# Performance work log

Hardware: AMD Instinct MI355X
Metric: run time of the kernel (lower is better)

## Reference

```python
import jax, jax.numpy as jnp
from jax import lax
import numpy as np

B, C, H, W = 16, 256, 96, 96
K = 11            # conv kernel size along one axis
C8 = C // 8       # query/key channels


def _conv(x, w, b):
    # 'same' conv in NCHW with OIHW weights; kernel is (kh,1) or (1,kw)
    kh, kw = w.shape[2], w.shape[3]
    y = lax.conv_general_dilated(
        x, w, window_strides=(1, 1),
        padding=((kh // 2, kh // 2), (kw // 2, kw // 2)),
        dimension_numbers=('NCHW', 'OIHW', 'NCHW'))
    return y + b[None, :, None, None]


def setup_inputs() -> dict:
    key = jax.random.key(0)
    ks = jax.random.split(key, 14)
    s = 0.05
    d = {
        'x':    jax.random.normal(ks[0], (B, C, H, W), jnp.float32),
        'wq_h': jax.random.normal(ks[1], (C8, C, K, 1), jnp.float32) * s,
        'bq_h': jax.random.normal(ks[2], (C8,), jnp.float32) * s,
        'wq_w': jax.random.normal(ks[3], (C8, C, 1, K), jnp.float32) * s,
        'bq_w': jax.random.normal(ks[4], (C8,), jnp.float32) * s,
        'wk_h': jax.random.normal(ks[5], (C8, C, K, 1), jnp.float32) * s,
        'bk_h': jax.random.normal(ks[6], (C8,), jnp.float32) * s,
        'wk_w': jax.random.normal(ks[7], (C8, C, 1, K), jnp.float32) * s,
        'bk_w': jax.random.normal(ks[8], (C8,), jnp.float32) * s,
        'wv_h': jax.random.normal(ks[9], (C, C, K, 1), jnp.float32) * s,
        'bv_h': jax.random.normal(ks[10], (C,), jnp.float32) * s,
        'wv_w': jax.random.normal(ks[11], (C, C, 1, K), jnp.float32) * s,
        'bv_w': jax.random.normal(ks[12], (C,), jnp.float32) * s,
        # gamma is a learned scalar (zero-init in torch); nonzero here so the
        # attention path contributes to the output
        'gamma': jax.random.normal(ks[13], (1,), jnp.float32) * 0.5,
    }
    return d


def reference(x, wq_h, bq_h, wq_w, bq_w, wk_h, bk_h, wk_w, bk_w,
              wv_h, bv_h, wv_w, bv_w, gamma):
    b, c, h, w = x.shape
    q_h = _conv(x, wq_h, bq_h)   # [B, C8, H, W]
    q_w = _conv(x, wq_w, bq_w)
    k_h = _conv(x, wk_h, bk_h)
    k_w = _conv(x, wk_w, bk_w)
    v_h = _conv(x, wv_h, bv_h)   # [B, C, H, W]
    v_w = _conv(x, wv_w, bv_w)
    # column (H-axis) attention energies: [B, H, W, H'] with -inf on h==h'
    e_h = jnp.einsum('bchw,bcHw->bhwH', q_h, k_h)
    diag = jnp.eye(h, dtype=bool)[None, :, None, :]  # [1, H, 1, H']
    e_h = jnp.where(diag, -jnp.inf, e_h)
    # row (W-axis) attention energies: [B, H, W, W']
    e_w = jnp.einsum('bchw,bchW->bhwW', q_w, k_w)
    # joint softmax over concatenated H'+W' axis
    att = jax.nn.softmax(jnp.concatenate([e_h, e_w], axis=-1), axis=-1)
    a_h = att[..., :h]           # [B, H, W, H']
    a_w = att[..., h:]           # [B, H, W, W']
    out_h = jnp.einsum('bcHw,bhwH->bchw', v_h, a_h)
    out_w = jnp.einsum('bchW,bhwW->bchw', v_w, a_w)
    return gamma * (out_h + out_w) + x
```

## Files before the change

### kernel.cpp

```cpp
#include <hip/hip_runtime.h>

constexpr int Bn = 16, Cn = 256, Hn = 96, Wn = 96, Pn = Hn * Wn;

#define DI static __device__ __forceinline__

struct alignas(16) U4 { unsigned a, b, c, d; };

typedef _Float16 f16x8 __attribute__((ext_vector_type(8)));
typedef float f32x4 __attribute__((ext_vector_type(4)));

#define GLOAD16(g, l) __builtin_amdgcn_global_load_lds( \
    (const __attribute__((address_space(1))) void*)(g), \
    (__attribute__((address_space(3))) void*)(l), 16, 0, 0)

__global__ void k_wt16(const float* __restrict__ w, _Float16* __restrict__ wt,
                       int co_n, int co_off, int co_tot) {
    int idx = blockIdx.x * 256 + threadIdx.x;
    if (idx >= co_n * 2816) return;
    int co = idx / 2816;
    int r  = idx - co * 2816;
    int c  = r / 11, t = r - c * 11;
    wt[((size_t)t * co_tot + co_off + co) * 256 + c] = (_Float16)w[idx];
}

__global__ __launch_bounds__(256) void k_xsplit(const float* __restrict__ x,
                                                _Float16* __restrict__ xh, _Float16* __restrict__ xl,
                                                _Float16* __restrict__ xhT, _Float16* __restrict__ xlT) {
    int b = blockIdx.y;
    int tid = threadIdx.x;
    int p = blockIdx.x * 128 + (tid >> 1);
    int half = tid & 1;
    int h = p / 96, w = p - h * 96;
    int pT = w * 96 + h;
    const float* xb = x + (size_t)b * Cn * Pn + p;
    size_t ob  = ((size_t)b * Pn + p) * 256;
    size_t obT = ((size_t)b * Pn + pT) * 256;
    for (int it = 0; it < 16; ++it) {
        int c0 = it * 16 + half * 8;
        f16x8 vh_, vl_;
#pragma unroll
        for (int i = 0; i < 8; ++i) {
            float f = xb[(size_t)(c0 + i) * Pn];
            _Float16 hh = (_Float16)f;
            vh_[i] = hh;
            vl_[i] = (_Float16)(f - (float)hh);
        }
        *(f16x8*)(xh + ob + c0) = vh_;
        *(f16x8*)(xl + ob + c0) = vl_;
        *(f16x8*)(xhT + obT + c0) = vh_;
        *(f16x8*)(xlT + obT + c0) = vl_;
    }
}

__global__ __launch_bounds__(256, 2) void k_conv_v(const _Float16* __restrict__ X0,
                                                   const _Float16* __restrict__ W0,
                                                   const float* __restrict__ b0a,
                                                   _Float16* __restrict__ o0,
                                                   const _Float16* __restrict__ X1,
                                                   const _Float16* __restrict__ W1,
                                                   const float* __restrict__ b1a,
                                                   _Float16* __restrict__ o1) {
    __shared__ char sm_raw[57344];
    const int tid = threadIdx.x;
    const int lane = tid & 63, wave = tid >> 6;
    const int wm = wave >> 1, wn = wave & 1;
    const int l15 = lane & 15, kg = lane >> 4;
    int fid = blockIdx.x + 24 * (blockIdx.y + 4 * blockIdx.z);
    int swz = (fid & 7) * 384 + (fid >> 3);
    const int bx = swz % 24;
    int rest = swz / 24;
    const int co0 = (rest & 3) * 64;
    const int z = rest >> 2;
    const int fam = z >> 4, b = z & 15;
    const _Float16* X  = fam ? X1 : X0;
    const _Float16* WT = fam ? W1 : W0;
    const float* bias  = fam ? b1a : b0a;
    _Float16* out      = fam ? o1 : o0;

    for (int zz = tid; zz < 2048; zz += 256) {
        int bufo = (zz >> 10) * 28672;
        int s = (zz >> 7) & 7, off = zz & 127;
        int Rbase = (s >> 1) * 112 + ((s & 1) ? 104 : 0);
        *(unsigned*)(sm_raw + bufo + Rbase * 64 + off * 4) = 0u;
    }

    f32x4 acc[2][12];
#pragma unroll
    for (int mf = 0; mf < 2; ++mf) {
        const float* bp = bias + co0 + wm * 32 + mf * 16 + kg * 4;
        f32x4 bv = { bp[0], bp[1], bp[2], bp[3] };
#pragma unroll
        for (int j = 0; j < 12; ++j) acc[mf][j] = bv;
    }

    const _Float16* Xb = X + ((size_t)b * Pn + bx * 384) * 256;
    const _Float16* Wb = WT + (size_t)(co0 + wm * 32 + l15) * 256 + kg * 8;

    auto STAGE = [&](int c0, int bufo) {
        for (int i = wave; i < 24; i += 4) {
            int s = i / 6, wch = i - s * 6;
            int row_local = 8 + wch * 16 + (lane >> 2);
            int kchunk = (lane & 3) ^ ((row_local >> 1) & 3);
            const _Float16* src = Xb + ((size_t)(s * 96 + row_local - 8)) * 256 + c0 + kchunk * 8;
            char* dst = sm_raw + bufo + (s * 112 + 8 + wch * 16) * 64;
            GLOAD16(src, dst);
        }
    };
    auto LDA = [&](f16x8* slot, const _Float16* tp) {
#pragma unroll
        for (int mf = 0; mf < 2; ++mf) slot[mf] = *(const f16x8*)(tp + mf * 4096);
    };
    auto LDB = [&](f16x8* dst, const char* Bb, int T) {
        int rl0 = 3 + l15 + T;
        const char* bp = Bb + (wn * 224 + rl0) * 64 + ((kg ^ ((rl0 >> 1) & 3)) << 4);
#pragma unroll
        for (int s = 0; s < 2; ++s)
#pragma unroll
            for (int nf = 0; nf < 6; ++nf)
                dst[s * 6 + nf] = *(const f16x8*)(bp + s * 7168 + nf * 1024);
    };

    STAGE(0, 0);
    __syncthreads();

    int cur = 0;
    for (int s8 = 0; s8 < 8; ++s8) {
        const int c0 = s8 * 32;
        const _Float16* wc = Wb + c0;
        f16x8 afc[2], afn[2];
        LDA(afc, wc);
        if (s8 < 7) STAGE(c0 + 32, (cur ^ 1) * 28672);
        const char* Bb = sm_raw + cur * 28672;
        f16x8 bf[12];
#pragma unroll
        for (int t = 0; t < 11; ++t) {
            if (t < 10) LDA(afn, wc + (t + 1) * 65536);
            LDB(bf, Bb, t);
            __builtin_amdgcn_s_setprio(1);
#pragma unroll
            for (int mf = 0; mf < 2; ++mf)
#pragma unroll
                for (int j = 0; j < 12; ++j)
                    acc[mf][j] = __builtin_amdgcn_mfma_f32_16x16x32_f16(afc[mf], bf[j], acc[mf][j], 0, 0, 0);
            __builtin_amdgcn_s_setprio(0);
            if (t < 10) {
#pragma unroll
                for (int mf = 0; mf < 2; ++mf) afc[mf] = afn[mf];
            }
        }
        __syncthreads();
        cur ^= 1;
    }

    _Float16* sb = (_Float16*)sm_raw;
#pragma unroll
    for (int mf = 0; mf < 2; ++mf)
#pragma unroll
        for (int j = 0; j < 12; ++j)
#pragma unroll
            for (int r = 0; r < 4; ++r) {
                int row = wm * 32 + mf * 16 + kg * 4 + r;
                int p = wn * 192 + (j / 6) * 96 + (j % 6) * 16 + l15;
                sb[row * 384 + p] = (_Float16)acc[mf][j][r];
            }
    __syncthreads();
    for (int k = 0; k < 12; ++k) {
        int ci = tid + k * 256;
        int row = ci / 48, ch = ci - row * 48;
        U4 v = *(const U4*)(sm_raw + row * 768 + ch * 16);
        *(U4*)(out + ((size_t)b * 256 + co0 + row) * Pn + bx * 384 + ch * 8) = v;
    }
}

__global__ __launch_bounds__(256, 2) void k_conv_qk(const _Float16* __restrict__ Xh0,
                                                    const _Float16* __restrict__ Xl0,
                                                    const _Float16* __restrict__ W0,
                                                    const float* __restrict__ bq0, const float* __restrict__ bk0,
                                                    _Float16* __restrict__ q0, _Float16* __restrict__ k0,
                                                    const _Float16* __restrict__ Xh1,
                                                    const _Float16* __restrict__ Xl1,
                                                    const _Float16* __restrict__ W1,
                                                    const float* __restrict__ bq1, const float* __restrict__ bk1,
                                                    _Float16* __restrict__ q1, _Float16* __restrict__ k1) {
    __shared__ char sm_raw[57344];
    const int tid = threadIdx.x;
    const int lane = tid & 63, wave = tid >> 6;
    const int wm = wave >> 1, wn = wave & 1;
    const int l15 = lane & 15, kg = lane >> 4;
    int fid = blockIdx.x + 48 * blockIdx.z;
    int swz = (fid & 7) * 192 + (fid >> 3);
    const int bx = swz % 48;
    const int zz0 = swz / 48;
    const int fam = zz0 >> 4, b = zz0 & 15;
    const _Float16* Xh = fam ? Xh1 : Xh0;
    const _Float16* Xl = fam ? Xl1 : Xl0;
    const _Float16* WT = fam ? W1 : W0;
    const float* bq = fam ? bq1 : bq0;
    const float* bk = fam ? bk1 : bk0;
    _Float16* q16 = fam ? q1 : q0;
    _Float16* k16 = fam ? k1 : k0;

    for (int z = tid; z < 2048; z += 256) {
        int bufo = (z >> 10) * 28672;
        int s = (z >> 7) & 7, off = z & 127;
        int Rbase = (s >> 1) * 112 + ((s & 1) ? 104 : 0);
        *(unsigned*)(sm_raw + bufo + Rbase * 64 + off * 4) = 0u;
    }

    f32x4 acc[2][6];
#pragma unroll
    for (int mf = 0; mf < 2; ++mf) {
        int cb = wm * 32 + mf * 16 + kg * 4;
        f32x4 bv;
#pragma unroll
        for (int r = 0; r < 4; ++r) {
            int co_l = cb + r;
            bv[r] = (co_l < 32) ? bq[co_l] : bk[co_l - 32];
        }
#pragma unroll
        for (int nf = 0; nf < 6; ++nf) acc[mf][nf] = bv;
    }

    const _Float16* Xbh = Xh + ((size_t)b * Pn + bx * 192) * 256;
    const _Float16* Xbl = Xl + ((size_t)b * Pn + bx * 192) * 256;
    const _Float16* Wb = WT + (size_t)(wm * 32 + l15) * 256 + kg * 8;

    auto STAGE = [&](int c0, int bufo) {
        for (int i = wave; i < 24; i += 4) {
            int a = i / 12, rr = (i / 6) & 1, wch = i % 6;
            int row_local = 8 + wch * 16 + (lane >> 2);
            int kchunk = (lane & 3) ^ ((row_local >> 1) & 3);
            const _Float16* base = (a == 0) ? Xbh : Xbl;
            const _Float16* src = base + ((size_t)(rr * 96 + row_local - 8)) * 256 + c0 + kchunk * 8;
            char* dst = sm_raw + bufo + ((a * 2 + rr) * 112 + 8 + wch * 16) * 64;
            GLOAD16(src, dst);
        }
    };
    auto LDBHL = [&](f16x8* dh, f16x8* dl, const char* Bb, int T) {
        int rl0 = 3 + l15 + T;
        const char* bp = Bb + (wn * 112 + rl0) * 64 + ((kg ^ ((rl0 >> 1) & 3)) << 4);
#pragma unroll
        for (int nf = 0; nf < 6; ++nf) {
            dh[nf] = *(const f16x8*)(bp + nf * 1024);
            dl[nf] = *(const f16x8*)(bp + 14336 + nf * 1024);
        }
    };

    STAGE(0, 0);
    __syncthreads();

    int cur = 0;
    for (int s8 = 0; s8 < 8; ++s8) {
        const int c0 = s8 * 32;
        const _Float16* wc = Wb + c0;
        f16x8 afc[2], afn[2];
#pragma unroll
        for (int mf = 0; mf < 2; ++mf) afc[mf] = *(const f16x8*)(wc + mf * 4096);
        if (s8 < 7) STAGE(c0 + 32, (cur ^ 1) * 28672);
        const char* Bb = sm_raw + cur * 28672;
#pragma unroll
        for (int t = 0; t < 11; ++t) {
            if (t < 10) {
#pragma unroll
                for (int mf = 0; mf < 2; ++mf)
                    afn[mf] = *(const f16x8*)(wc + (t + 1) * 16384 + mf * 4096);
            }
            f16x8 bh[6], bl[6];
            LDBHL(bh, bl, Bb, t);
            __builtin_amdgcn_s_setprio(1);
#pragma unroll
            for (int mf = 0; mf < 2; ++mf)
#pragma unroll
                for (int nf = 0; nf < 6; ++nf) {
                    acc[mf][nf] = __builtin_amdgcn_mfma_f32_16x16x32_f16(afc[mf], bh[nf], acc[mf][nf], 0, 0, 0);
                    acc[mf][nf] = __builtin_amdgcn_mfma_f32_16x16x32_f16(afc[mf], bl[nf], acc[mf][nf], 0, 0, 0);
                }
            __builtin_amdgcn_s_setprio(0);
            if (t < 10) {
#pragma unroll
                for (int mf = 0; mf < 2; ++mf) afc[mf] = afn[mf];
            }
        }
        __syncthreads();
        cur ^= 1;
    }

    __syncthreads();
    _Float16* sq = (_Float16*)sm_raw;
    _Float16* sk = (_Float16*)(sm_raw + 12288);
#pragma unroll
    for (int mf = 0; mf < 2; ++mf) {
        int cb = wm * 32 + mf * 16 + kg * 4;
#pragma unroll
        for (int r = 0; r < 4; ++r) {
            int co_l = cb + r;
            _Float16* arr = (co_l < 32) ? sq : sk;
            int c = co_l & 31;
#pragma unroll
            for (int nf = 0; nf < 6; ++nf) {
                int p = wn * 96 + nf * 16 + l15;
                arr[p * 32 + c] = (_Float16)acc[mf][nf][r];
            }
        }
    }
    __syncthreads();
    for (int j = 0; j < 6; ++j) {
        int idx = tid + j * 256;
        int mtx = idx >= 768;
        int e = idx - mtx * 768;
        int p = e >> 2, cg2 = e & 3;
        U4 v = *(const U4*)(sm_raw + mtx * 12288 + p * 64 + cg2 * 16);
        _Float16* dstb = mtx ? k16 : q16;
        *(U4*)(dstb + ((size_t)b * Pn + bx * 192 + p) * 32 + cg2 * 8) = v;
    }
}

DI void stage_qk16(const _Float16* qg, const _Float16* kg, char* Lq, char* Lk, int tid) {
    for (int i = tid; i < 768; i += 256) {
        int mtx = i >= 384;
        int e = i - mtx * 384;
        int p = e >> 2, ch = e & 3;
        const _Float16* src = (mtx ? kg : qg) + p * 32 + ch * 8;
        f16x8 v = *(const f16x8*)src;
        char* dst = (mtx ? Lk : Lq) + p * 64 + ((ch ^ ((p >> 1) & 3)) << 4);
        *(f16x8*)dst = v;
    }
}

DI void mfma_e(const char* Lq, const char* Lk, float* Ef, int lane, int wave) {
    int l15 = lane & 15, kg = lane >> 4;
    int wm = wave >> 1, wn = wave & 1;
    f16x8 qa[3], kb[3];
#pragma unroll
    for (int i = 0; i < 3; ++i) {
        int pr = wm * 48 + i * 16 + l15;
        qa[i] = *(const f16x8*)(Lq + pr * 64 + ((kg ^ ((pr >> 1) & 3)) << 4));
        int pc = wn * 48 + i * 16 + l15;
        kb[i] = *(const f16x8*)(Lk + pc * 64 + ((kg ^ ((pc >> 1) & 3)) << 4));
    }
#pragma unroll
    for (int i = 0; i < 3; ++i)
#pragma unroll
        for (int j = 0; j < 3; ++j) {
            f32x4 a = { 0.f, 0.f, 0.f, 0.f };
            a = __builtin_amdgcn_mfma_f32_16x16x32_f16(qa[i], kb[j], a, 0, 0, 0);
#pragma unroll
            for (int r = 0; r < 4; ++r) {
                int row = wm * 48 + i * 16 + kg * 4 + r;
                int col = wn * 48 + j * 16 + l15;
                Ef[row * 97 + col] = a[r];
            }
        }
}

__global__ __launch_bounds__(256) void k_p1(const _Float16* __restrict__ q16, const _Float16* __restrict__ k16,
                                            float* __restrict__ mh, float* __restrict__ lh) {
    __shared__ char L[49536];
    float* Ef = (float*)L;
    char* Lq = L + 37248;
    char* Lk = L + 43392;
    const int tid = threadIdx.x, lane = tid & 63, wave = tid >> 6;
    const int w = blockIdx.x, b = blockIdx.y;
    const _Float16* qg = q16 + ((size_t)b * Pn + w * 96) * 32;
    const _Float16* kg = k16 + ((size_t)b * Pn + w * 96) * 32;
    stage_qk16(qg, kg, Lq, Lk, tid);
    __syncthreads();
    mfma_e(Lq, Lk, Ef, lane, wave);
    __syncthreads();
    if (tid < 96) {
        int h = tid;
        const float* er = Ef + h * 97;
        float m = -INFINITY;
        for (int j = 0; j < 96; ++j) if (j != h) m = fmaxf(m, er[j]);
        float l = 0.f;
        for (int j = 0; j < 96; ++j) if (j != h) l += __expf(er[j] - m);
        mh[((size_t)b * 96 + w) * 96 + h] = m;
        lh[((size_t)b * 96 + w) * 96 + h] = l;
    }
}

__global__ __launch_bounds__(256) void k_p2(const _Float16* __restrict__ q16, const _Float16* __restrict__ k16,
                                            const _Float16* __restrict__ V,
                                            const float* __restrict__ mh, const float* __restrict__ lh,
                                            float* __restrict__ mo, float* __restrict__ lo,
                                            _Float16* __restrict__ outw) {
    __shared__ char L[56448];
    float* Ef = (float*)L;
    char* LA  = L + 37248;
    char* Lq  = L + 37248;
    char* Lk  = L + 43392;
    float* Marr = (float*)(L + 55680);
    float* Linv = (float*)(L + 56064);
    const int tid = threadIdx.x, lane = tid & 63, wave = tid >> 6;
    const int l15 = lane & 15, kg = lane >> 4;
    const int h = blockIdx.x, b = blockIdx.y;
    const _Float16* qg = q16 + ((size_t)b * Pn + h * 96) * 32;
    const _Float16* kgp = k16 + ((size_t)b * Pn + h * 96) * 32;
    stage_qk16(qg, kgp, Lq, Lk, tid);
    __syncthreads();
    mfma_e(Lq, Lk, Ef, lane, wave);
    __syncthreads();
    if (tid < 96) {
        int wq = tid;
        const float* er = Ef + wq * 97;
        float mw = -INFINITY;
        for (int j = 0; j < 96; ++j) mw = fmaxf(mw, er[j]);
        float lw = 0.f;
        for (int j = 0; j < 96; ++j) lw += __expf(er[j] - mw);
        float mhv = mh[((size_t)b * 96 + wq) * 96 + h];
        float lhv = lh[((size_t)b * 96 + wq) * 96 + h];
        float m = fmaxf(mhv, mw);
        float l = lhv * __expf(mhv - m) + lw * __expf(mw - m);
        mo[((size_t)b * 96 + h) * 96 + wq] = m;
        lo[((size_t)b * 96 + h) * 96 + wq] = l;
        Marr[wq] = m;
        Linv[wq] = 1.f / l;
    }
    __syncthreads();
    if (tid < 192) {
        int r = tid >> 1, half = tid & 1;
        float m = Marr[r], li = Linv[r];
        const float* er = Ef + r * 97;
        for (int cc = 0; cc < 6; ++cc) {
            int chunk = half * 6 + cc;
            f16x8 av;
#pragma unroll
            for (int jj = 0; jj < 8; ++jj)
                av[jj] = (_Float16)(__expf(er[chunk * 8 + jj] - m) * li);
            *(f16x8*)(LA + r * 192 + ((chunk ^ ((r >> 1) & 3)) << 4)) = av;
        }
    }
    __syncthreads();
    f32x4 acc[4][6];
#pragma unroll
    for (int mf = 0; mf < 4; ++mf)
#pragma unroll
        for (int nf = 0; nf < 6; ++nf) acc[mf][nf] = f32x4{ 0.f, 0.f, 0.f, 0.f };
    const _Float16* vb = V + ((size_t)b * 256 + wave * 64 + l15) * Pn + h * 96 + kg * 8;
    f16x8 va[4][3];
#pragma unroll
    for (int mf = 0; mf < 4; ++mf)
#pragma unroll
        for (int ks = 0; ks < 3; ++ks)
            va[mf][ks] = *(const f16x8*)(vb + (size_t)mf * 16 * Pn + ks * 32);
#pragma unroll
    for (int ks = 0; ks < 3; ++ks)
#pragma unroll
        for (int nf = 0; nf < 6; ++nf) {
            int wq = nf * 16 + l15;
            int chunk = ks * 4 + kg;
            f16x8 bv = *(const f16x8*)(LA + wq * 192 + ((chunk ^ ((wq >> 1) & 3)) << 4));
#pragma unroll
            for (int mf = 0; mf < 4; ++mf)
                acc[mf][nf] = __builtin_amdgcn_mfma_f32_16x16x32_f16(va[mf][ks], bv, acc[mf][nf], 0, 0, 0);
        }
    _Float16* ob = outw + ((size_t)b * 256) * Pn + h * 96;
#pragma unroll
    for (int mf = 0; mf < 4; ++mf)
#pragma unroll
        for (int nf = 0; nf < 6; ++nf)
#pragma unroll
            for (int r = 0; r < 4; ++r) {
                int c = wave * 64 + mf * 16 + kg * 4 + r;
                ob[(size_t)c * Pn + nf * 16 + l15] = (_Float16)acc[mf][nf][r];
            }
}

__global__ __launch_bounds__(256) void k_p3(const _Float16* __restrict__ q16, const _Float16* __restrict__ k16,
                                            const _Float16* __restrict__ V,
                                            const float* __restrict__ mo, const float* __restrict__ lo,
                                            _Float16* __restrict__ pT) {
    __shared__ char L[56448];
    float* Ef = (float*)L;
    char* LA  = L + 37248;
    char* Lq  = L + 37248;
    char* Lk  = L + 43392;
    float* Marr = (float*)(L + 55680);
    float* Linv = (float*)(L + 56064);
    const int tid = threadIdx.x, lane = tid & 63, wave = tid >> 6;
    const int l15 = lane & 15, kg = lane >> 4;
    const int w = blockIdx.x, b = blockIdx.y;
    const _Float16* qg = q16 + ((size_t)b * Pn + w * 96) * 32;
    const _Float16* kgp = k16 + ((size_t)b * Pn + w * 96) * 32;
    stage_qk16(qg, kgp, Lq, Lk, tid);
    __syncthreads();
    mfma_e(Lq, Lk, Ef, lane, wave);
    __syncthreads();
    if (tid < 96) {
        int hq = tid;
        Marr[hq] = mo[((size_t)b * 96 + hq) * 96 + w];
        Linv[hq] = 1.f / lo[((size_t)b * 96 + hq) * 96 + w];
    }
    __syncthreads();
    if (tid < 192) {
        int r = tid >> 1, half = tid & 1;
        float m = Marr[r], li = Linv[r];
        const float* er = Ef + r * 97;
        for (int cc = 0; cc < 6; ++cc) {
            int chunk = half * 6 + cc;
            f16x8 av;
#pragma unroll
            for (int jj = 0; jj < 8; ++jj) {
                int col = chunk * 8 + jj;
                av[jj] = (col == r) ? (_Float16)0.f
                                    : (_Float16)(__expf(er[col] - m) * li);
            }
            *(f16x8*)(LA + r * 192 + ((chunk ^ ((r >> 1) & 3)) << 4)) = av;
        }
    }
    __syncthreads();
    f32x4 acc[4][6];
#pragma unroll
    for (int mf = 0; mf < 4; ++mf)
#pragma unroll
        for (int nf = 0; nf < 6; ++nf) acc[mf][nf] = f32x4{ 0.f, 0.f, 0.f, 0.f };
    const _Float16* vb = V + ((size_t)b * 256 + wave * 64 + l15) * Pn + w * 96 + kg * 8;
    f16x8 va[4][3];
#pragma unroll
    for (int mf = 0; mf < 4; ++mf)
#pragma unroll
        for (int ks = 0; ks < 3; ++ks)
            va[mf][ks] = *(const f16x8*)(vb + (size_t)mf * 16 * Pn + ks * 32);
#pragma unroll
    for (int ks = 0; ks < 3; ++ks)
#pragma unroll
        for (int nf = 0; nf < 6; ++nf) {
            int hq = nf * 16 + l15;
            int chunk = ks * 4 + kg;
            f16x8 bv = *(const f16x8*)(LA + hq * 192 + ((chunk ^ ((hq >> 1) & 3)) << 4));
#pragma unroll
            for (int mf = 0; mf < 4; ++mf)
                acc[mf][nf] = __builtin_amdgcn_mfma_f32_16x16x32_f16(va[mf][ks], bv, acc[mf][nf], 0, 0, 0);
        }
    _Float16* pb = pT + ((size_t)b * 256) * Pn + w * 96;
#pragma unroll
    for (int mf = 0; mf < 4; ++mf)
#pragma unroll
        for (int nf = 0; nf < 6; ++nf)
#pragma unroll
            for (int r = 0; r < 4; ++r) {
                int c = wave * 64 + mf * 16 + kg * 4 + r;
                pb[(size_t)c * Pn + nf * 16 + l15] = (_Float16)acc[mf][nf][r];
            }
}

__global__ __launch_bounds__(256) void k_combine(const _Float16* __restrict__ pT,
                                                 const _Float16* __restrict__ ow,
                                                 const float* __restrict__ x,
                                                 const float* __restrict__ gamma,
                                                 float* __restrict__ out) {
    __shared__ float T[32][33];
    int bh = blockIdx.x, bw = blockIdx.y;
    size_t ib = (size_t)blockIdx.z * Pn;
    int tx = threadIdx.x, ty = threadIdx.y;
#pragma unroll
    for (int i = 0; i < 4; ++i) {
        int r = bw * 32 + ty + i * 8;
        T[ty + i * 8][tx] = (float)pT[ib + (size_t)r * 96 + bh * 32 + tx];
    }
    __syncthreads();
    float g = gamma[0];
#pragma unroll
    for (int i = 0; i < 4; ++i) {
        int hh = bh * 32 + ty + i * 8, ww = bw * 32 + tx;
        size_t o = ib + (size_t)hh * 96 + ww;
        out[o] = g * (T[tx][ty + i * 8] + (float)ow[o]) + x[o];
    }
}

extern "C" void kernel_launch(void* const* d_in, const int* in_sizes, int n_in,
                              void* d_out, int out_size, void* d_ws, size_t ws_size,
                              hipStream_t stream) {
    (void)in_sizes; (void)n_in; (void)out_size; (void)ws_size;
    const float* x   = (const float*)d_in[0];
    const float* wqh = (const float*)d_in[1];
    const float* bqh = (const float*)d_in[2];
    const float* wqw = (const float*)d_in[3];
    const float* bqw = (const float*)d_in[4];
    const float* wkh = (const float*)d_in[5];
    const float* bkh = (const float*)d_in[6];
    const float* wkw = (const float*)d_in[7];
    const float* bkw = (const float*)d_in[8];
    const float* wvh = (const float*)d_in[9];
    const float* bvh = (const float*)d_in[10];
    const float* wvw = (const float*)d_in[11];
    const float* bvw = (const float*)d_in[12];
    const float* gam = (const float*)d_in[13];
    float* out = (float*)d_out;

    char* ws = (char*)d_ws;
    size_t off = 0;
    auto alloc = [&](size_t bytes) -> char* {
        char* p = ws + off;
        off = (off + bytes + 255) & ~(size_t)255;
        return p;
    };
    const size_t IMG = (size_t)Bn * Cn * Pn;
    const size_t QK16 = (size_t)Bn * Pn * 32;

    _Float16* xh  = (_Float16*)alloc(IMG * 2);
    _Float16* xl  = (_Float16*)alloc(IMG * 2);
    _Float16* xhT = (_Float16*)alloc(IMG * 2);
    _Float16* xlT = (_Float16*)alloc(IMG * 2);
    _Float16* qh16 = (_Float16*)alloc(QK16 * 2);
    _Float16* kh16 = (_Float16*)alloc(QK16 * 2);
    _Float16* qw16 = (_Float16*)alloc(QK16 * 2);
    _Float16* kw16 = (_Float16*)alloc(QK16 * 2);
    float* mh = (float*)alloc((size_t)Bn * Pn * 4);
    float* lh = (float*)alloc((size_t)Bn * Pn * 4);
    float* mo = (float*)alloc((size_t)Bn * Pn * 4);
    float* lo = (float*)alloc((size_t)Bn * Pn * 4);
    _Float16* wqkh  = (_Float16*)alloc((size_t)11 * 64 * 256 * 2);
    _Float16* wqkw  = (_Float16*)alloc((size_t)11 * 64 * 256 * 2);
    _Float16* wvh16 = (_Float16*)alloc((size_t)11 * 256 * 256 * 2);
    _Float16* wvw16 = (_Float16*)alloc((size_t)11 * 256 * 256 * 2);
    _Float16* vh = xlT;
    _Float16* vw = xl;
    _Float16* pT = xhT;
    _Float16* ow16 = xh;

    const int gq = (32 * 2816 + 255) / 256;
    const int gv = (256 * 2816 + 255) / 256;
    k_wt16<<<gq, 256, 0, stream>>>(wqh, wqkh, 32, 0, 64);
    k_wt16<<<gq, 256, 0, stream>>>(wkh, wqkh, 32, 32, 64);
    k_wt16<<<gq, 256, 0, stream>>>(wqw, wqkw, 32, 0, 64);
    k_wt16<<<gq, 256, 0, stream>>>(wkw, wqkw, 32, 32, 64);
    k_wt16<<<gv, 256, 0, stream>>>(wvh, wvh16, 256, 0, 256);
    k_wt16<<<gv, 256, 0, stream>>>(wvw, wvw16, 256, 0, 256);

    k_xsplit<<<dim3(72, 16), 256, 0, stream>>>(x, xh, xl, xhT, xlT);

    k_conv_qk<<<dim3(48, 1, 32), 256, 0, stream>>>(xhT, xlT, wqkh, bqh, bkh, qh16, kh16,
                                                   xh,  xl,  wqkw, bqw, bkw, qw16, kw16);
    k_conv_v <<<dim3(24, 4, 32), 256, 0, stream>>>(xhT, wvh16, bvh, vh,
                                                   xh,  wvw16, bvw, vw);

    k_p1<<<dim3(96, 16), 256, 0, stream>>>(qh16, kh16, mh, lh);
    k_p2<<<dim3(96, 16), 256, 0, stream>>>(qw16, kw16, vw, mh, lh, mo, lo, ow16);
    k_p3<<<dim3(96, 16), 256, 0, stream>>>(qh16, kh16, vh, mo, lo, pT);

    k_combine<<<dim3(3, 3, Bn * Cn), dim3(32, 8), 0, stream>>>(pT, ow16, x, gam, out);
}
```

Before: 988.5 us.

## Split softmax row reductions across two threads and reorder conv block mapping

The row max/sum-exp reductions in the two attention-energy kernels now use 192 threads, each handling half a row, with partial results combined through shared memory scratch that reuses the staged q/k buffers. The diagonal mask in the column pass becomes a -inf write into the energy tile instead of a per-element branch. The value-conv kernel's swizzled block index now takes the output-channel tile from the low bits, so blocks that share the same input tile run close together. This adds extra barriers and shared-memory traffic in exchange for more parallel reduction work and better input reuse.

New measurement: 968.0 us, median of 2. 1.02x faster.

```diff
diff --git a/kernel.cpp b/kernel.cpp
--- a/kernel.cpp
+++ b/kernel.cpp
@@ -67,10 +67,10 @@
     const int l15 = lane & 15, kg = lane >> 4;
     int fid = blockIdx.x + 24 * (blockIdx.y + 4 * blockIdx.z);
     int swz = (fid & 7) * 384 + (fid >> 3);
-    const int bx = swz % 24;
-    int rest = swz / 24;
-    const int co0 = (rest & 3) * 64;
-    const int z = rest >> 2;
+    const int co0 = (swz & 3) * 64;
+    int rest = swz >> 2;
+    const int bx = rest % 24;
+    const int z = rest / 24;
     const int fam = z >> 4, b = z & 15;
     const _Float16* X  = fam ? X1 : X0;
     const _Float16* WT = fam ? W1 : W0;
@@ -367,15 +367,30 @@
     __syncthreads();
     mfma_e(Lq, Lk, Ef, lane, wave);
     __syncthreads();
+    if (tid < 96) Ef[tid * 97 + tid] = -INFINITY;
+    __syncthreads();
+    float* red  = (float*)Lq;
+    float* red2 = red + 192;
+    if (tid < 192) {
+        int r = tid >> 1, hf = tid & 1;
+        const float* er = Ef + r * 97 + hf * 48;
+        float m = -INFINITY;
+        for (int j = 0; j < 48; ++j) m = fmaxf(m, er[j]);
+        red[tid] = m;
+    }
+    __syncthreads();
+    if (tid < 192) {
+        int r = tid >> 1, hf = tid & 1;
+        float m = fmaxf(red[r * 2], red[r * 2 + 1]);
+        const float* er = Ef + r * 97 + hf * 48;
+        float s = 0.f;
+        for (int j = 0; j < 48; ++j) s += __expf(er[j] - m);
+        red2[tid] = s;
+    }
+    __syncthreads();
     if (tid < 96) {
-        int h = tid;
-        const float* er = Ef + h * 97;
-        float m = -INFINITY;
-        for (int j = 0; j < 96; ++j) if (j != h) m = fmaxf(m, er[j]);
-        float l = 0.f;
-        for (int j = 0; j < 96; ++j) if (j != h) l += __expf(er[j] - m);
-        mh[((size_t)b * 96 + w) * 96 + h] = m;
-        lh[((size_t)b * 96 + w) * 96 + h] = l;
+        mh[((size_t)b * 96 + w) * 96 + tid] = fmaxf(red[tid * 2], red[tid * 2 + 1]);
+        lh[((size_t)b * 96 + w) * 96 + tid] = red2[tid * 2] + red2[tid * 2 + 1];
     }
 }
 
@@ -400,13 +415,29 @@
     __syncthreads();
     mfma_e(Lq, Lk, Ef, lane, wave);
     __syncthreads();
+    float* red  = (float*)Lk;
+    float* red2 = red + 192;
+    if (tid < 192) {
+        int r = tid >> 1, hf = tid & 1;
+        const float* er = Ef + r * 97 + hf * 48;
+        float m = -INFINITY;
+        for (int j = 0; j < 48; ++j) m = fmaxf(m, er[j]);
+        red[tid] = m;
+    }
+    __syncthreads();
+    if (tid < 192) {
+        int r = tid >> 1, hf = tid & 1;
+        float m = fmaxf(red[r * 2], red[r * 2 + 1]);
+        const float* er = Ef + r * 97 + hf * 48;
+        float s = 0.f;
+        for (int j = 0; j < 48; ++j) s += __expf(er[j] - m);
+        red2[tid] = s;
+    }
+    __syncthreads();
     if (tid < 96) {
         int wq = tid;
-        const float* er = Ef + wq * 97;
-        float mw = -INFINITY;
-        for (int j = 0; j < 96; ++j) mw = fmaxf(mw, er[j]);
-        float lw = 0.f;
-        for (int j = 0; j < 96; ++j) lw += __expf(er[j] - mw);
+        float mw = fmaxf(red[wq * 2], red[wq * 2 + 1]);
+        float lw = red2[wq * 2] + red2[wq * 2 + 1];
         float mhv = mh[((size_t)b * 96 + wq) * 96 + h];
         float lhv = lh[((size_t)b * 96 + wq) * 96 + h];
         float m = fmaxf(mhv, mw);
```
